# Kernel tuning notes

Hardware: AMD Instinct MI355X
Metric: run time of the kernel (lower is better)

## Reference

```python
import jax, jax.numpy as jnp
import numpy as np

HEADS = 8
DIM_HEAD = 64
SCALE = DIM_HEAD ** -0.5


def setup_inputs() -> dict:
    key = jax.random.key(0)
    ks = jax.random.split(key, 6)
    B, N, D = 1, 4096, 640
    INNER = HEADS * DIM_HEAD  # 512
    s = lambda fan_in: 1.0 / np.sqrt(fan_in)
    return {
        "x": jax.random.normal(ks[0], (B, N, D), dtype=jnp.float32),
        "Wq": jax.random.normal(ks[1], (D, INNER), dtype=jnp.float32) * s(D),
        "Wk": jax.random.normal(ks[2], (D, INNER), dtype=jnp.float32) * s(D),
        "Wv": jax.random.normal(ks[3], (D, INNER), dtype=jnp.float32) * s(D),
        "Wo": jax.random.normal(ks[4], (INNER, D), dtype=jnp.float32) * s(INNER),
        "bo": jnp.zeros((D,), dtype=jnp.float32),
    }


def reference(x, Wq, Wk, Wv, Wo, bo):
    B, N, _ = x.shape
    h, d = HEADS, DIM_HEAD
    # self-attention: context = x
    q = (x @ Wq).reshape(B, N, h, d).transpose(0, 2, 1, 3)  # [B,h,N,d]
    k = (x @ Wk).reshape(B, N, h, d).transpose(0, 2, 1, 3)
    v = (x @ Wv).reshape(B, N, h, d).transpose(0, 2, 1, 3)
    sim = jnp.einsum('bhid,bhjd->bhij', q, k) * SCALE  # [B,h,N,N]
    attn = jax.nn.softmax(sim, axis=-1)
    out = jnp.einsum('bhij,bhjd->bhid', attn, v)  # [B,h,N,d]
    out = out.transpose(0, 2, 1, 3).reshape(B, N, h * d)  # [B,N,inner]
    return out @ Wo + bo  # dropout p=0.0 is identity
```

## Files before the change

### kernel.cpp

```cpp
#include <hip/hip_runtime.h>
#include <math.h>

#define NSEQ   4096
#define DMODEL 640
#define NHEAD  8
#define DHEAD  64
#define INNER  512
#define KVSPLIT 2

typedef _Float16 f16;
typedef _Float16 f16x8 __attribute__((ext_vector_type(8)));
typedef _Float16 f16x4 __attribute__((ext_vector_type(4)));
typedef float    f32x4 __attribute__((ext_vector_type(4)));

#define MFMA16(a, b, c) __builtin_amdgcn_mfma_f32_16x16x32_f16((a), (b), (c), 0, 0, 0)

#define QSCALE 0.18033688011112042f

__device__ __forceinline__ void gl16(const f16* g, f16* l) {
    __builtin_amdgcn_global_load_lds(
        (const __attribute__((address_space(1))) unsigned int*)g,
        (__attribute__((address_space(3))) unsigned int*)l, 16, 0, 0);
}

__global__ __launch_bounds__(256) void cvt_x(const float* __restrict__ x,
                                             f16* __restrict__ xh) {
    int i = (blockIdx.x * 256 + threadIdx.x) * 8;
    float4 a = *(const float4*)&x[i];
    float4 b = *(const float4*)&x[i + 4];
    f16x8 o = {(f16)a.x, (f16)a.y, (f16)a.z, (f16)a.w,
               (f16)b.x, (f16)b.y, (f16)b.z, (f16)b.w};
    *(f16x8*)&xh[i] = o;
}

__global__ __launch_bounds__(256) void transpose_cvt3(
    const float* __restrict__ Wq, const float* __restrict__ Wk,
    const float* __restrict__ Wv,
    f16* __restrict__ WTq, f16* __restrict__ WTk, f16* __restrict__ WTv) {
    __shared__ __align__(16) f16 T[64][72];
    const float* src = blockIdx.z == 0 ? Wq : blockIdx.z == 1 ? Wk : Wv;
    f16* dst = blockIdx.z == 0 ? WTq : blockIdx.z == 1 ? WTk : WTv;
    const int R = DMODEL, C = INNER;
    const int c0 = blockIdx.x * 64, r0 = blockIdx.y * 64;
    const int t = threadIdx.x;
    {
        int r = t >> 2, cb = (t & 3) * 16;
#pragma unroll
        for (int i = 0; i < 16; i += 4) {
            float4 v = *(const float4*)&src[(size_t)(r0 + r) * C + c0 + cb + i];
            T[cb + i + 0][r] = (f16)v.x;
            T[cb + i + 1][r] = (f16)v.y;
            T[cb + i + 2][r] = (f16)v.z;
            T[cb + i + 3][r] = (f16)v.w;
        }
    }
    __syncthreads();
    {
        int c = t >> 2, rb = (t & 3) * 16;
        f16* d = dst + (size_t)(c0 + c) * R + r0 + rb;
        *(f16x8*)d = *(const f16x8*)&T[c][rb];
        *(f16x8*)(d + 8) = *(const f16x8*)&T[c][rb + 8];
    }
}

__global__ __launch_bounds__(256) void transpose_cvt(
    const float* __restrict__ src, f16* __restrict__ dst, int R, int C) {
    __shared__ __align__(16) f16 T[64][72];
    const int c0 = blockIdx.x * 64, r0 = blockIdx.y * 64;
    const int t = threadIdx.x;
    {
        int r = t >> 2, cb = (t & 3) * 16;
#pragma unroll
        for (int i = 0; i < 16; i += 4) {
            float4 v = *(const float4*)&src[(size_t)(r0 + r) * C + c0 + cb + i];
            T[cb + i + 0][r] = (f16)v.x;
            T[cb + i + 1][r] = (f16)v.y;
            T[cb + i + 2][r] = (f16)v.z;
            T[cb + i + 3][r] = (f16)v.w;
        }
    }
    __syncthreads();
    {
        int c = t >> 2, rb = (t & 3) * 16;
        f16* d = dst + (size_t)(c0 + c) * R + r0 + rb;
        *(f16x8*)d = *(const f16x8*)&T[c][rb];
        *(f16x8*)(d + 8) = *(const f16x8*)&T[c][rb + 8];
    }
}

__global__ __launch_bounds__(256) void qkv_gemm16(
    const f16* __restrict__ xh,
    const f16* __restrict__ WTq, const f16* __restrict__ WTk,
    const f16* __restrict__ WTv,
    f16* __restrict__ q16, f16* __restrict__ k16, f16* __restrict__ vT16)
{
    __shared__ __align__(16) f16 Xs[4096];
    __shared__ __align__(16) f16 Ws[4096];
    __shared__ __align__(16) f16 Cs[64][72];

    const int bx = blockIdx.x;
    const int by = blockIdx.y;
    const int bz = blockIdx.z;
    const f16* WT = (bz == 0) ? WTq : (bz == 1) ? WTk : WTv;

    const int tid = threadIdx.x;
    const int w = tid >> 6, lane = tid & 63;
    const int lr = lane & 15, lc = lane >> 4;
    const int srow8 = lane >> 3;
    const int le = 8 * ((lane & 7) ^ srow8);
    const int swz0 = 8 * (lc ^ (lr & 7));
    const int swz1 = 8 * ((lc + 4) ^ (lr & 7));
    const int m0 = by * 64, n0 = bx * 64;

    f32x4 acc[4] = {};

    for (int s = 0; s < DMODEL / 64; ++s) {
        const int k0 = s * 64;
#pragma unroll
        for (int c = 0; c < 2; ++c) {
            const int cc = w * 2 + c;
            gl16(xh + (size_t)(m0 + cc * 8 + srow8) * DMODEL + k0 + le,
                 &Xs[cc * 512]);
            gl16(WT + (size_t)(n0 + cc * 8 + srow8) * DMODEL + k0 + le,
                 &Ws[cc * 512]);
        }
        __syncthreads();
        f16x8 a0 = *(const f16x8*)&Xs[(16 * w + lr) * 64 + swz0];
        f16x8 a1 = *(const f16x8*)&Xs[(16 * w + lr) * 64 + swz1];
#pragma unroll
        for (int nt = 0; nt < 4; ++nt) {
            f16x8 b0 = *(const f16x8*)&Ws[(nt * 16 + lr) * 64 + swz0];
            f16x8 b1 = *(const f16x8*)&Ws[(nt * 16 + lr) * 64 + swz1];
            acc[nt] = MFMA16(a1, b1, MFMA16(a0, b0, acc[nt]));
        }
        __syncthreads();
    }

    const float sc = (bz == 0) ? QSCALE : 1.0f;
    if (bz < 2) {
#pragma unroll
        for (int nt = 0; nt < 4; ++nt)
#pragma unroll
            for (int r = 0; r < 4; ++r)
                Cs[16 * w + lc * 4 + r][nt * 16 + lr] = (f16)(acc[nt][r] * sc);
    } else {
#pragma unroll
        for (int nt = 0; nt < 4; ++nt)
#pragma unroll
            for (int r = 0; r < 4; ++r)
                Cs[nt * 16 + lr][16 * w + lc * 4 + r] = (f16)acc[nt][r];
    }
    __syncthreads();
    {
        const int rr = tid >> 2, cb = (tid & 3) * 16;
        f16x8 v0 = *(const f16x8*)&Cs[rr][cb];
        f16x8 v1 = *(const f16x8*)&Cs[rr][cb + 8];
        f16* dst;
        if (bz == 0)
            dst = q16 + ((size_t)bx * NSEQ + m0 + rr) * DHEAD + cb;
        else if (bz == 1)
            dst = k16 + ((size_t)bx * NSEQ + m0 + rr) * DHEAD + cb;
        else
            dst = vT16 + ((size_t)bx * DHEAD + rr) * NSEQ + m0 + cb;
        *(f16x8*)dst = v0;
        *(f16x8*)(dst + 8) = v1;
    }
}

__global__ __launch_bounds__(256, 2) void attn_fwd(
    const f16* __restrict__ q16, const f16* __restrict__ k16,
    const f16* __restrict__ vT16, f16* __restrict__ Opart,
    float* __restrict__ Ml)
{
    __shared__ __align__(16) f16 KsB[2][4096];
    __shared__ __align__(16) f16 VtB[2][4096];
    __shared__ __align__(16) f16 Ps[8192];

    const int lin = blockIdx.x + 32 * blockIdx.y + 256 * blockIdx.z;
    const int h  = lin & 7;
    const int qb = (lin >> 3) & 31;
    const int sp = lin >> 8;

    const int tid = threadIdx.x;
    const int w = tid >> 6, lane = tid & 63;
    const int lr = lane & 15, lc = lane >> 4;
    const int srow8 = lane >> 3;
    const int le = 8 * ((lane & 7) ^ srow8);
    const int swz0 = 8 * (lc ^ (lr & 7));
    const int swz1 = 8 * ((lc + 4) ^ (lr & 7));

    const f16* kp = k16 + ((size_t)h * NSEQ + sp * (NSEQ / KVSPLIT)) * DHEAD;
    const f16* vp = vT16 + (size_t)h * DHEAD * NSEQ + sp * (NSEQ / KVSPLIT);

    f16x8 qf[2][2];
#pragma unroll
    for (int g = 0; g < 2; ++g) {
        const f16* qp = q16 +
            ((size_t)h * NSEQ + qb * 128 + 32 * w + 16 * g + lr) * DHEAD;
        qf[g][0] = *(const f16x8*)&qp[lc * 8];
        qf[g][1] = *(const f16x8*)&qp[32 + lc * 8];
    }

    float m_run[2] = {-INFINITY, -INFINITY}, l_run[2] = {0.f, 0.f};
    f32x4 o[2][4] = {};

#pragma unroll
    for (int c = 0; c < 2; ++c) {
        const int cc = 2 * w + c;
        gl16(kp + (size_t)(cc * 8 + srow8) * DHEAD + le, &KsB[0][cc * 512]);
        gl16(vp + (size_t)(cc * 8 + srow8) * NSEQ + le, &VtB[0][cc * 512]);
    }
    __syncthreads();

    const int NT = NSEQ / KVSPLIT / 64;
    for (int kt = 0; kt < NT; ++kt) {
        const int cur = kt & 1;
        if (kt < NT - 1) {
            const int nb = cur ^ 1;
#pragma unroll
            for (int c = 0; c < 2; ++c) {
                const int cc = 2 * w + c;
                gl16(kp + (size_t)((kt + 1) * 64 + cc * 8 + srow8) * DHEAD + le,
                     &KsB[nb][cc * 512]);
                gl16(vp + (size_t)(cc * 8 + srow8) * NSEQ + (kt + 1) * 64 + le,
                     &VtB[nb][cc * 512]);
            }
        }

        f32x4 s[2][4];
        const f32x4 z4 = {0.f, 0.f, 0.f, 0.f};
#pragma unroll
        for (int t = 0; t < 4; ++t) {
            f16x8 ka = *(const f16x8*)&KsB[cur][(t * 16 + lr) * 64 + swz0];
            f16x8 kb = *(const f16x8*)&KsB[cur][(t * 16 + lr) * 64 + swz1];
#pragma unroll
            for (int g = 0; g < 2; ++g)
                s[g][t] = MFMA16(kb, qf[g][1], MFMA16(ka, qf[g][0], z4));
        }

        float pm[2];
#pragma unroll
        for (int g = 0; g < 2; ++g) {
            float m = s[g][0][0];
#pragma unroll
            for (int t = 0; t < 4; ++t)
#pragma unroll
                for (int r = 0; r < 4; ++r) m = fmaxf(m, s[g][t][r]);
            m = fmaxf(m, __shfl_xor(m, 16));
            m = fmaxf(m, __shfl_xor(m, 32));
            pm[g] = m;
        }
        if (__any((pm[0] > m_run[0]) | (pm[1] > m_run[1]))) {
#pragma unroll
            for (int g = 0; g < 2; ++g) {
                const float mn = fmaxf(m_run[g], pm[g]);
                const float al = __builtin_amdgcn_exp2f(m_run[g] - mn);
                m_run[g] = mn;
                l_run[g] *= al;
#pragma unroll
                for (int dt = 0; dt < 4; ++dt) o[g][dt] *= al;
            }
        }
#pragma unroll
        for (int g = 0; g < 2; ++g) {
            float ps = 0.f;
#pragma unroll
            for (int t = 0; t < 4; ++t)
#pragma unroll
                for (int r = 0; r < 4; ++r) {
                    s[g][t][r] = __builtin_amdgcn_exp2f(s[g][t][r] - m_run[g]);
                    ps += s[g][t][r];
                }
            ps += __shfl_xor(ps, 16);
            ps += __shfl_xor(ps, 32);
            l_run[g] += ps;
        }

#pragma unroll
        for (int g = 0; g < 2; ++g) {
            const int row = 32 * w + 16 * g + lr;
#pragma unroll
            for (int t = 0; t < 4; ++t) {
                f16x4 pk = {(f16)s[g][t][0], (f16)s[g][t][1],
                            (f16)s[g][t][2], (f16)s[g][t][3]};
                const int col = (16 * t + 4 * lc) ^ ((lr & 7) << 3);
                *(f16x4*)&Ps[row * 64 + col] = pk;
            }
        }

        f16x8 pb[2][2];
#pragma unroll
        for (int g = 0; g < 2; ++g) {
            const int row = 32 * w + 16 * g + lr;
            pb[g][0] = *(const f16x8*)&Ps[row * 64 + swz0];
            pb[g][1] = *(const f16x8*)&Ps[row * 64 + swz1];
        }
#pragma unroll
        for (int dt = 0; dt < 4; ++dt) {
            f16x8 va0 = *(const f16x8*)&VtB[cur][(dt * 16 + lr) * 64 + swz0];
            f16x8 va1 = *(const f16x8*)&VtB[cur][(dt * 16 + lr) * 64 + swz1];
#pragma unroll
            for (int g = 0; g < 2; ++g)
                o[g][dt] = MFMA16(va1, pb[g][1], MFMA16(va0, pb[g][0], o[g][dt]));
        }
        __syncthreads();
    }

#pragma unroll
    for (int g = 0; g < 2; ++g) {
        const float linv = 1.0f / l_run[g];
        const size_t qg = (size_t)qb * 128 + 32 * w + 16 * g + lr;
        f16* ob = Opart + (((size_t)(sp * 8 + h)) * NSEQ + qg) * DHEAD;
#pragma unroll
        for (int dt = 0; dt < 4; ++dt) {
            f16x4 ov = {(f16)(o[g][dt][0] * linv), (f16)(o[g][dt][1] * linv),
                        (f16)(o[g][dt][2] * linv), (f16)(o[g][dt][3] * linv)};
            *(f16x4*)&ob[dt * 16 + 4 * lc] = ov;
        }
        if (lc == 0) {
            float2 ml = make_float2(m_run[g], l_run[g]);
            *(float2*)&Ml[(((size_t)(sp * 8 + h)) * NSEQ + qg) * 2] = ml;
        }
    }
}

__global__ __launch_bounds__(256) void out_gemm16(
    const f16* __restrict__ Opart, const float* __restrict__ Ml,
    const f16* __restrict__ WoT,
    const float* __restrict__ bias, float* __restrict__ C)
{
    __shared__ __align__(16) f16 Xs[4096];
    __shared__ __align__(16) f16 Ws[4096];

    const int bx = blockIdx.x;
    const int by = blockIdx.y;
    const int tid = threadIdx.x;
    const int w = tid >> 6, lane = tid & 63;
    const int lr = lane & 15, lc = lane >> 4;
    const int srow8 = lane >> 3;
    const int j = lane & 7;
    const int le = 8 * (j ^ srow8);
    const int swz0 = 8 * (lc ^ (lr & 7));
    const int swz1 = 8 * ((lc + 4) ^ (lr & 7));
    const int m0 = by * 64, n0 = bx * 64;

    f32x4 acc[4] = {};

    for (int s8 = 0; s8 < 8; ++s8) {
        const int k0 = s8 * 64;
#pragma unroll
        for (int c = 0; c < 2; ++c) {
            const int cc = w * 2 + c;
            gl16(WoT + (size_t)(n0 + cc * 8 + srow8) * INNER + k0 + le,
                 &Ws[cc * 512]);
            const int row = cc * 8 + srow8;
            const size_t q = (size_t)m0 + row;
            f16x8 o0 = *(const f16x8*)&Opart[((size_t)s8 * NSEQ + q) * DHEAD + 8 * j];
            f16x8 o1 = *(const f16x8*)&Opart[((size_t)(8 + s8) * NSEQ + q) * DHEAD + 8 * j];
            float2 ml0 = *(const float2*)&Ml[((size_t)s8 * NSEQ + q) * 2];
            float2 ml1 = *(const float2*)&Ml[((size_t)(8 + s8) * NSEQ + q) * 2];
            const float mx = fmaxf(ml0.x, ml1.x);
            float w0 = ml0.y * __builtin_amdgcn_exp2f(ml0.x - mx);
            float w1 = ml1.y * __builtin_amdgcn_exp2f(ml1.x - mx);
            const float inv = 1.0f / (w0 + w1);
            w0 *= inv; w1 *= inv;
            f16x8 a8;
#pragma unroll
            for (int e = 0; e < 8; ++e)
                a8[e] = (f16)((float)o0[e] * w0 + (float)o1[e] * w1);
            *(f16x8*)&Xs[row * 64 + 8 * (j ^ (row & 7))] = a8;
        }
        __syncthreads();
        f16x8 a0 = *(const f16x8*)&Xs[(16 * w + lr) * 64 + swz0];
        f16x8 a1 = *(const f16x8*)&Xs[(16 * w + lr) * 64 + swz1];
#pragma unroll
        for (int nt = 0; nt < 4; ++nt) {
            f16x8 b0 = *(const f16x8*)&Ws[(nt * 16 + lr) * 64 + swz0];
            f16x8 b1 = *(const f16x8*)&Ws[(nt * 16 + lr) * 64 + swz1];
            acc[nt] = MFMA16(a1, b1, MFMA16(a0, b0, acc[nt]));
        }
        __syncthreads();
    }

#pragma unroll
    for (int nt = 0; nt < 4; ++nt) {
        const float b = bias[n0 + nt * 16 + lr];
#pragma unroll
        for (int r = 0; r < 4; ++r)
            C[(size_t)(m0 + 16 * w + lc * 4 + r) * DMODEL + n0 + nt * 16 + lr] =
                acc[nt][r] + b;
    }
}

extern "C" void kernel_launch(void* const* d_in, const int* in_sizes, int n_in,
                              void* d_out, int out_size, void* d_ws, size_t ws_size,
                              hipStream_t stream) {
    const float* x  = (const float*)d_in[0];
    const float* Wq = (const float*)d_in[1];
    const float* Wk = (const float*)d_in[2];
    const float* Wv = (const float*)d_in[3];
    const float* Wo = (const float*)d_in[4];
    const float* bo = (const float*)d_in[5];
    float* out = (float*)d_out;

    char* base = (char*)d_ws;
    f16*   Opart = (f16*)base;
    f16*   xh    = (f16*)base;
    f16*   WTq   = xh + (size_t)NSEQ * DMODEL;
    f16*   WTk   = WTq + (size_t)INNER * DMODEL;
    f16*   WTv   = WTk + (size_t)INNER * DMODEL;
    float* Ml    = (float*)(base + 8388608);
    f16*   WoT   = (f16*)(base + 8912896);
    f16*   q16   = (f16*)(base + 9568256);
    f16*   k16   = q16 + (size_t)NHEAD * NSEQ * DHEAD;
    f16*   vT16  = k16 + (size_t)NHEAD * NSEQ * DHEAD;

    cvt_x<<<NSEQ * DMODEL / (256 * 8), 256, 0, stream>>>(x, xh);
    transpose_cvt3<<<dim3(INNER / 64, DMODEL / 64, 3), 256, 0, stream>>>(
        Wq, Wk, Wv, WTq, WTk, WTv);
    transpose_cvt<<<dim3(DMODEL / 64, INNER / 64), 256, 0, stream>>>(
        Wo, WoT, INNER, DMODEL);

    qkv_gemm16<<<dim3(NHEAD, NSEQ / 64, 3), 256, 0, stream>>>(
        xh, WTq, WTk, WTv, q16, k16, vT16);
    attn_fwd<<<dim3(NSEQ / 128, NHEAD, KVSPLIT), 256, 0, stream>>>(
        q16, k16, vT16, Opart, Ml);
    out_gemm16<<<dim3(DMODEL / 64, NSEQ / 64), 256, 0, stream>>>(
        Opart, Ml, WoT, bo, out);
}
```

Baseline: 172.6 us.

## Double-buffer LDS tiles in QKV and output GEMMs, add MFMA priority hints

The QKV projection GEMM and the output GEMM now keep two LDS buffers and prefetch the next K-slice (and, in the output GEMM, the split-combine of the next slice) while MFMAs run on the current one. This removes one barrier per iteration and aims to hide global-load latency. The attention kernel brackets its two MFMA blocks with s_setprio to favour matrix issue. The cost is doubled LDS use per block, which can lower occupancy, and the Cs epilogue buffer now aliases Xs.

New measurement: 177.5 us. 1.03x slower.

```diff
diff --git a/kernel.cpp b/kernel.cpp
--- a/kernel.cpp
+++ b/kernel.cpp
@@ -94,9 +94,9 @@
     const f16* __restrict__ WTv,
     f16* __restrict__ q16, f16* __restrict__ k16, f16* __restrict__ vT16)
 {
-    __shared__ __align__(16) f16 Xs[4096];
-    __shared__ __align__(16) f16 Ws[4096];
-    __shared__ __align__(16) f16 Cs[64][72];
+    __shared__ __align__(16) f16 Xs[2][4096];
+    __shared__ __align__(16) f16 Ws[2][4096];
+    f16 (*Cs)[72] = (f16(*)[72])&Xs[0][0];
 
     const int bx = blockIdx.x;
     const int by = blockIdx.y;
@@ -114,23 +114,37 @@
 
     f32x4 acc[4] = {};
 
-    for (int s = 0; s < DMODEL / 64; ++s) {
-        const int k0 = s * 64;
-#pragma unroll
-        for (int c = 0; c < 2; ++c) {
-            const int cc = w * 2 + c;
-            gl16(xh + (size_t)(m0 + cc * 8 + srow8) * DMODEL + k0 + le,
-                 &Xs[cc * 512]);
-            gl16(WT + (size_t)(n0 + cc * 8 + srow8) * DMODEL + k0 + le,
-                 &Ws[cc * 512]);
-        }
-        __syncthreads();
-        f16x8 a0 = *(const f16x8*)&Xs[(16 * w + lr) * 64 + swz0];
-        f16x8 a1 = *(const f16x8*)&Xs[(16 * w + lr) * 64 + swz1];
+#pragma unroll
+    for (int c = 0; c < 2; ++c) {
+        const int cc = w * 2 + c;
+        gl16(xh + (size_t)(m0 + cc * 8 + srow8) * DMODEL + le,
+             &Xs[0][cc * 512]);
+        gl16(WT + (size_t)(n0 + cc * 8 + srow8) * DMODEL + le,
+             &Ws[0][cc * 512]);
+    }
+    __syncthreads();
+
+    const int NS = DMODEL / 64;
+    for (int s = 0; s < NS; ++s) {
+        const int cur = s & 1;
+        if (s < NS - 1) {
+            const int nb = cur ^ 1;
+            const int k0n = (s + 1) * 64;
+#pragma unroll
+            for (int c = 0; c < 2; ++c) {
+                const int cc = w * 2 + c;
+                gl16(xh + (size_t)(m0 + cc * 8 + srow8) * DMODEL + k0n + le,
+                     &Xs[nb][cc * 512]);
+                gl16(WT + (size_t)(n0 + cc * 8 + srow8) * DMODEL + k0n + le,
+                     &Ws[nb][cc * 512]);
+            }
+        }
+        f16x8 a0 = *(const f16x8*)&Xs[cur][(16 * w + lr) * 64 + swz0];
+        f16x8 a1 = *(const f16x8*)&Xs[cur][(16 * w + lr) * 64 + swz1];
 #pragma unroll
         for (int nt = 0; nt < 4; ++nt) {
-            f16x8 b0 = *(const f16x8*)&Ws[(nt * 16 + lr) * 64 + swz0];
-            f16x8 b1 = *(const f16x8*)&Ws[(nt * 16 + lr) * 64 + swz1];
+            f16x8 b0 = *(const f16x8*)&Ws[cur][(nt * 16 + lr) * 64 + swz0];
+            f16x8 b1 = *(const f16x8*)&Ws[cur][(nt * 16 + lr) * 64 + swz1];
             acc[nt] = MFMA16(a1, b1, MFMA16(a0, b0, acc[nt]));
         }
         __syncthreads();
@@ -229,6 +243,7 @@
 
         f32x4 s[2][4];
         const f32x4 z4 = {0.f, 0.f, 0.f, 0.f};
+        __builtin_amdgcn_s_setprio(1);
 #pragma unroll
         for (int t = 0; t < 4; ++t) {
             f16x8 ka = *(const f16x8*)&KsB[cur][(t * 16 + lr) * 64 + swz0];
@@ -237,6 +252,7 @@
             for (int g = 0; g < 2; ++g)
                 s[g][t] = MFMA16(kb, qf[g][1], MFMA16(ka, qf[g][0], z4));
         }
+        __builtin_amdgcn_s_setprio(0);
 
         float pm[2];
 #pragma unroll
@@ -295,6 +311,7 @@
             pb[g][0] = *(const f16x8*)&Ps[row * 64 + swz0];
             pb[g][1] = *(const f16x8*)&Ps[row * 64 + swz1];
         }
+        __builtin_amdgcn_s_setprio(1);
 #pragma unroll
         for (int dt = 0; dt < 4; ++dt) {
             f16x8 va0 = *(const f16x8*)&VtB[cur][(dt * 16 + lr) * 64 + swz0];
@@ -303,6 +320,7 @@
             for (int g = 0; g < 2; ++g)
                 o[g][dt] = MFMA16(va1, pb[g][1], MFMA16(va0, pb[g][0], o[g][dt]));
         }
+        __builtin_amdgcn_s_setprio(0);
         __syncthreads();
     }
 
@@ -329,8 +347,8 @@
     const f16* __restrict__ WoT,
     const float* __restrict__ bias, float* __restrict__ C)
 {
-    __shared__ __align__(16) f16 Xs[4096];
-    __shared__ __align__(16) f16 Ws[4096];
+    __shared__ __align__(16) f16 Xs[2][4096];
+    __shared__ __align__(16) f16 Ws[2][4096];
 
     const int bx = blockIdx.x;
     const int by = blockIdx.y;
@@ -344,40 +362,61 @@
     const int swz1 = 8 * ((lc + 4) ^ (lr & 7));
     const int m0 = by * 64, n0 = bx * 64;
 
+    const int row_c0 = (2 * w + 0) * 8 + srow8;
+    const int row_c1 = (2 * w + 1) * 8 + srow8;
+
     f32x4 acc[4] = {};
 
+    auto combine = [&](int s8, int row) -> f16x8 {
+        const size_t q = (size_t)m0 + row;
+        f16x8 o0 = *(const f16x8*)&Opart[((size_t)s8 * NSEQ + q) * DHEAD + 8 * j];
+        f16x8 o1 = *(const f16x8*)&Opart[((size_t)(8 + s8) * NSEQ + q) * DHEAD + 8 * j];
+        float2 ml0 = *(const float2*)&Ml[((size_t)s8 * NSEQ + q) * 2];
+        float2 ml1 = *(const float2*)&Ml[((size_t)(8 + s8) * NSEQ + q) * 2];
+        const float mx = fmaxf(ml0.x, ml1.x);
+        float w0 = ml0.y * __builtin_amdgcn_exp2f(ml0.x - mx);
+        float w1 = ml1.y * __builtin_amdgcn_exp2f(ml1.x - mx);
+        const float inv = 1.0f / (w0 + w1);
+        w0 *= inv; w1 *= inv;
+        f16x8 a8;
+#pragma unroll
+        for (int e = 0; e < 8; ++e)
+            a8[e] = (f16)((float)o0[e] * w0 + (float)o1[e] * w1);
+        return a8;
+    };
+
+    gl16(WoT + (size_t)(n0 + row_c0) * INNER + le, &Ws[0][(2 * w + 0) * 512]);
+    gl16(WoT + (size_t)(n0 + row_c1) * INNER + le, &Ws[0][(2 * w + 1) * 512]);
+    *(f16x8*)&Xs[0][row_c0 * 64 + 8 * (j ^ (row_c0 & 7))] = combine(0, row_c0);
+    *(f16x8*)&Xs[0][row_c1 * 64 + 8 * (j ^ (row_c1 & 7))] = combine(0, row_c1);
+    __syncthreads();
+
     for (int s8 = 0; s8 < 8; ++s8) {
-        const int k0 = s8 * 64;
-#pragma unroll
-        for (int c = 0; c < 2; ++c) {
-            const int cc = w * 2 + c;
-            gl16(WoT + (size_t)(n0 + cc * 8 + srow8) * INNER + k0 + le,
-                 &Ws[cc * 512]);
-            const int row = cc * 8 + srow8;
-            const size_t q = (size_t)m0 + row;
-            f16x8 o0 = *(const f16x8*)&Opart[((size_t)s8 * NSEQ + q) * DHEAD + 8 * j];
-            f16x8 o1 = *(const f16x8*)&Opart[((size_t)(8 + s8) * NSEQ + q) * DHEAD + 8 * j];
-            float2 ml0 = *(const float2*)&Ml[((size_t)s8 * NSEQ + q) * 2];
-            float2 ml1 = *(const float2*)&Ml[((size_t)(8 + s8) * NSEQ + q) * 2];
-            const float mx = fmaxf(ml0.x, ml1.x);
-            float w0 = ml0.y * __builtin_amdgcn_exp2f(ml0.x - mx);
-            float w1 = ml1.y * __builtin_amdgcn_exp2f(ml1.x - mx);
-            const float inv = 1.0f / (w0 + w1);
-            w0 *= inv; w1 *= inv;
-            f16x8 a8;
-#pragma unroll
-            for (int e = 0; e < 8; ++e)
-                a8[e] = (f16)((float)o0[e] * w0 + (float)o1[e] * w1);
-            *(f16x8*)&Xs[row * 64 + 8 * (j ^ (row & 7))] = a8;
-        }
-        __syncthreads();
-        f16x8 a0 = *(const f16x8*)&Xs[(16 * w + lr) * 64 + swz0];
-        f16x8 a1 = *(const f16x8*)&Xs[(16 * w + lr) * 64 + swz1];
+        const int cur = s8 & 1;
+        f16x8 a8n_0, a8n_1;
+        const bool pre = (s8 < 7);
+        if (pre) {
+            const int nb = cur ^ 1;
+            const int k0n = (s8 + 1) * 64;
+            gl16(WoT + (size_t)(n0 + row_c0) * INNER + k0n + le,
+                 &Ws[nb][(2 * w + 0) * 512]);
+            gl16(WoT + (size_t)(n0 + row_c1) * INNER + k0n + le,
+                 &Ws[nb][(2 * w + 1) * 512]);
+            a8n_0 = combine(s8 + 1, row_c0);
+            a8n_1 = combine(s8 + 1, row_c1);
+        }
+        f16x8 a0 = *(const f16x8*)&Xs[cur][(16 * w + lr) * 64 + swz0];
+        f16x8 a1 = *(const f16x8*)&Xs[cur][(16 * w + lr) * 64 + swz1];
 #pragma unroll
         for (int nt = 0; nt < 4; ++nt) {
-            f16x8 b0 = *(const f16x8*)&Ws[(nt * 16 + lr) * 64 + swz0];
-            f16x8 b1 = *(const f16x8*)&Ws[(nt * 16 + lr) * 64 + swz1];
+            f16x8 b0 = *(const f16x8*)&Ws[cur][(nt * 16 + lr) * 64 + swz0];
+            f16x8 b1 = *(const f16x8*)&Ws[cur][(nt * 16 + lr) * 64 + swz1];
             acc[nt] = MFMA16(a1, b1, MFMA16(a0, b0, acc[nt]));
+        }
+        if (pre) {
+            const int nb = cur ^ 1;
+            *(f16x8*)&Xs[nb][row_c0 * 64 + 8 * (j ^ (row_c0 & 7))] = a8n_0;
+            *(f16x8*)&Xs[nb][row_c1 * 64 + 8 * (j ^ (row_c1 & 7))] = a8n_1;
         }
         __syncthreads();
     }
```
